# Optimization experiments

Hardware: AMD Instinct MI355X
Metric: run time of the kernel (lower is better)

Reference implementation:

```python
import jax, jax.numpy as jnp
import numpy as np
import hashlib

HIDDEN = 256
IN_SIZE = 32
ROUNDS = 64
BATCH = 8192


def _sha256_noise(nonces_u8: np.ndarray) -> np.ndarray:
    # Faithful to generate_noise: sha256 of the 32 nonce bytes gives 256 bits;
    # only indices i < 256 (byte_idx < 32) are set, so only round 0 has noise.
    B = nonces_u8.shape[0]
    noise = np.zeros((B, ROUNDS, HIDDEN), dtype=np.float32)
    for b in range(B):
        h = hashlib.sha256(nonces_u8[b].tobytes()).digest()
        bits = np.unpackbits(np.frombuffer(h, dtype=np.uint8), bitorder='little')
        noise[b, 0, :] = bits.astype(np.float32)
    return noise


def setup_inputs() -> dict:
    key = jax.random.key(0)
    k_nonce, k_mat = jax.random.split(key)
    nonces = jax.random.randint(k_nonce, (BATCH, IN_SIZE), 0, 256, dtype=jnp.int32)
    # Ternary round matrices in {-1, 0, 1}; original derives them from a
    # ChaCha20 keystream mod 3 minus 1 -- same distribution, different PRNG.
    matrices = (jax.random.randint(k_mat, (ROUNDS, HIDDEN, HIDDEN), 0, 3, dtype=jnp.int32) - 1).astype(jnp.float32)
    nonces_u8 = np.asarray(nonces).astype(np.uint8)
    noise = jnp.asarray(_sha256_noise(nonces_u8))  # [B, ROUNDS, HIDDEN]
    return {"nonces": nonces, "matrices": matrices, "noise": noise}


def reference(nonces, matrices, noise):
    B = nonces.shape[0]
    # Vectorized bit-unpack: x[b, i*8 + j] = (nonces[b, i] >> j) & 1
    bits = ((nonces[:, :, None] >> jnp.arange(8, dtype=jnp.int32)) & 1)
    x = bits.reshape(B, IN_SIZE * 8).astype(jnp.float32)  # [B, 256]

    noise_r = jnp.swapaxes(noise, 0, 1)  # [ROUNDS, B, HIDDEN]

    def step(x, mn):
        M, n = mn
        # torch: fmod(matmul(M, x.T).T + noise_r, 2.0) == fmod(x @ M.T + n, 2)
        return jnp.fmod(x @ M.T + n, 2.0), None

    x, _ = jax.lax.scan(step, x, (matrices, noise_r))
    return x
```

## Files before the change

kernel.cpp:

```cpp
#include <hip/hip_runtime.h>


#define HIDDEN 256
#define ROUNDS 64
#define ROWS_PER_BLOCK 32

typedef __attribute__((ext_vector_type(4))) int int4v;

struct alignas(16) C16 { char b[16]; };

__global__ void prep_B(const float* __restrict__ M, char* __restrict__ Bfrag) {
    int cid = blockIdx.x * blockDim.x + threadIdx.x;
    int lane = cid & 63;
    int q    = (cid >> 6) & 3;
    int t    = (cid >> 8) & 15;
    int r    = cid >> 12;
    int h  = 16 * t + (lane & 15);
    int k0 = 64 * q + (lane >> 4) * 16;
    const float* src = M + (((size_t)r * 256 + h) * 256 + k0);
    C16 w;
#pragma unroll
    for (int j = 0; j < 16; j++) w.b[j] = (char)src[j];
    *(C16*)(Bfrag + (size_t)cid * 16) = w;
}

__global__ __launch_bounds__(512, 2) void tenshash_main(
    const int*   __restrict__ nonces,
    const char*  __restrict__ Bfrag,
    const float* __restrict__ noise,
    float*       __restrict__ out)
{
    __shared__ alignas(16) char xbuf[2][ROWS_PER_BLOCK * HIDDEN];

    const int tid  = threadIdx.x;
    const int lane = tid & 63;
    const int wave = tid >> 6;
    const int lane15 = lane & 15;
    const int quad   = lane >> 4;
    const int b0 = blockIdx.x * ROWS_PER_BLOCK;

    {
        int m = tid >> 4;
        int c = tid & 15;
        int n0 = nonces[(b0 + m) * 32 + 2 * c];
        int n1 = nonces[(b0 + m) * 32 + 2 * c + 1];
        C16 w;
#pragma unroll
        for (int j = 0; j < 8; j++) w.b[j]     = (char)((n0 >> j) & 1);
#pragma unroll
        for (int j = 0; j < 8; j++) w.b[8 + j] = (char)((n1 >> j) & 1);
        int off = m * 256 + ((c ^ (m & 15)) * 16);
        *(C16*)&xbuf[0][off] = w;
    }
    __syncthreads();

    for (int r = 0; r < ROUNDS; r++) {
        const char* xcur = xbuf[r & 1];
        char*       xnxt = xbuf[(r & 1) ^ 1];

        int4v a[2][4];
#pragma unroll
        for (int mt = 0; mt < 2; mt++) {
            int m = 16 * mt + lane15;
#pragma unroll
            for (int kt = 0; kt < 4; kt++) {
                int c = 4 * kt + quad;
                int off = m * 256 + ((c ^ lane15) * 16);
                a[mt][kt] = *(const int4v*)&xcur[off];
            }
        }

        int4v acc[2][2];
#pragma unroll
        for (int nt = 0; nt < 2; nt++) {
            int t = wave * 2 + nt;
            const int4v* bptr = (const int4v*)Bfrag
                              + (((size_t)r * 16 + t) * 4) * 64 + lane;
            int4v b[4];
#pragma unroll
            for (int q = 0; q < 4; q++) b[q] = bptr[q * 64];
#pragma unroll
            for (int mt = 0; mt < 2; mt++) {
                int4v c = {0, 0, 0, 0};
#pragma unroll
                for (int q = 0; q < 4; q++)
                    c = __builtin_amdgcn_mfma_i32_16x16x64_i8(a[mt][q], b[q], c, 0, 0, 0);
                acc[nt][mt] = c;
            }
        }

#pragma unroll
        for (int nt = 0; nt < 2; nt++) {
            int t = wave * 2 + nt;
            int h = 16 * t + lane15;
#pragma unroll
            for (int mt = 0; mt < 2; mt++) {
#pragma unroll
                for (int reg = 0; reg < 4; reg++) {
                    int row = 16 * mt + 4 * quad + reg;
                    int v = acc[nt][mt][reg];
                    if (r == 0)
                        v += (int)noise[(size_t)(b0 + row) * (ROUNDS * 256) + h];
                    int m2 = v % 2;
                    if (r < ROUNDS - 1) {
                        int off = row * 256 + ((t ^ (row & 15)) * 16) + lane15;
                        xnxt[off] = (char)m2;
                    } else {
                        out[(size_t)(b0 + row) * 256 + h] = (float)m2;
                    }
                }
            }
        }
        __syncthreads();
    }
}

extern "C" void kernel_launch(void* const* d_in, const int* in_sizes, int n_in,
                              void* d_out, int out_size, void* d_ws, size_t ws_size,
                              hipStream_t stream) {
    const int*   nonces   = (const int*)d_in[0];
    const float* matrices = (const float*)d_in[1];
    const float* noise    = (const float*)d_in[2];
    float* out = (float*)d_out;
    char* Bfrag = (char*)d_ws;

    prep_B<<<1024, 256, 0, stream>>>(matrices, Bfrag);
    tenshash_main<<<256, 512, 0, stream>>>(nonces, Bfrag, noise, out);
}
```

Baseline: 654.4 us.

## Prefetch next-round matrix fragments into registers and swap MFMA operand roles

The main loop now loads the next round's ternary matrix fragments from global memory into a second register set while the current round's MFMAs run, double-buffering them across an unrolled pair of rounds. The matrix becomes the A operand and the activations the B operand, so each lane's output holds four consecutive hidden values. That lets results be written to shared memory as packed 32-bit stores, and the final output and round-0 noise as float4 vectors, instead of scalar byte and float accesses. prep_A also reads the source floats as float4. Holding the extra fragments costs more registers, which may strain the 2-blocks-per-CU launch bound.

```diff
diff --git a/kernel.cpp b/kernel.cpp
--- a/kernel.cpp
+++ b/kernel.cpp
@@ -1,43 +1,121 @@
 #include <hip/hip_runtime.h>
 
 
-#define HIDDEN 256
 #define ROUNDS 64
-#define ROWS_PER_BLOCK 32
+#define ROWS   32
 
-typedef __attribute__((ext_vector_type(4))) int int4v;
+typedef __attribute__((ext_vector_type(4))) int    int4v;
+typedef __attribute__((ext_vector_type(4))) float  float4v;
 
 struct alignas(16) C16 { char b[16]; };
 
-__global__ void prep_B(const float* __restrict__ M, char* __restrict__ Bfrag) {
-    int cid = blockIdx.x * blockDim.x + threadIdx.x;
+__global__ void prep_A(const float* __restrict__ M, char* __restrict__ A) {
+    int cid  = blockIdx.x * blockDim.x + threadIdx.x;
     int lane = cid & 63;
-    int q    = (cid >> 6) & 3;
-    int t    = (cid >> 8) & 15;
+    int kt   = (cid >> 6) & 3;
+    int ht   = (cid >> 8) & 15;
     int r    = cid >> 12;
-    int h  = 16 * t + (lane & 15);
-    int k0 = 64 * q + (lane >> 4) * 16;
-    const float* src = M + (((size_t)r * 256 + h) * 256 + k0);
+    int h  = 16 * ht + (lane & 15);
+    int k0 = 64 * kt + (lane >> 4) * 16;
+    const float4v* src = (const float4v*)(M + ((size_t)(r * 256 + h) * 256 + k0));
     C16 w;
 #pragma unroll
-    for (int j = 0; j < 16; j++) w.b[j] = (char)src[j];
-    *(C16*)(Bfrag + (size_t)cid * 16) = w;
+    for (int p = 0; p < 4; p++) {
+        float4v f = src[p];
+#pragma unroll
+        for (int e = 0; e < 4; e++) w.b[4 * p + e] = (char)f[e];
+    }
+    *(C16*)(A + (size_t)cid * 16) = w;
+}
+
+__device__ __forceinline__ void round_body(
+    int r, bool last, bool pre,
+    const char* __restrict__ xc, char* __restrict__ xn,
+    int4v (&a)[2][4], int4v (&an)[2][4],
+    const int4v* __restrict__ Abase,
+    const float* __restrict__ noise, float* __restrict__ out,
+    int b0, int lane, int wave)
+{
+    const int l15  = lane & 15;
+    const int quad = lane >> 4;
+
+    int4v b[2][4];
+#pragma unroll
+    for (int bt = 0; bt < 2; bt++) {
+        int row = 16 * bt + l15;
+#pragma unroll
+        for (int kt = 0; kt < 4; kt++) {
+            int c = 4 * kt + quad;
+            b[bt][kt] = *(const int4v*)&xc[row * 256 + ((c ^ l15) * 16)];
+        }
+    }
+
+    if (pre) {
+#pragma unroll
+        for (int i = 0; i < 2; i++) {
+            int ht = 2 * wave + i;
+#pragma unroll
+            for (int kt = 0; kt < 4; kt++)
+                an[i][kt] = Abase[(size_t)((((r + 1) * 16 + ht) * 4 + kt) * 64) + lane];
+        }
+    }
+
+    int4v acc[2][2];
+#pragma unroll
+    for (int i = 0; i < 2; i++)
+#pragma unroll
+        for (int bt = 0; bt < 2; bt++) {
+            int4v c = {0, 0, 0, 0};
+#pragma unroll
+            for (int kt = 0; kt < 4; kt++)
+                c = __builtin_amdgcn_mfma_i32_16x16x64_i8(a[i][kt], b[bt][kt], c, 0, 0, 0);
+            acc[i][bt] = c;
+        }
+
+#pragma unroll
+    for (int i = 0; i < 2; i++) {
+        int ht = 2 * wave + i;
+#pragma unroll
+        for (int bt = 0; bt < 2; bt++) {
+            int bb = 16 * bt + l15;
+            int4v v = acc[i][bt];
+            if (r == 0) {
+                float4v nz = *(const float4v*)&noise[(size_t)(b0 + bb) * (ROUNDS * 256)
+                                                     + 16 * ht + 4 * quad];
+#pragma unroll
+                for (int e = 0; e < 4; e++) v[e] += (int)nz[e];
+            }
+            if (!last) {
+                unsigned p = 0;
+#pragma unroll
+                for (int e = 0; e < 4; e++) {
+                    int m2 = v[e] % 2;
+                    p |= ((unsigned)(m2 & 0xff)) << (8 * e);
+                }
+                *(unsigned*)&xn[bb * 256 + ((ht ^ l15) * 16) + 4 * quad] = p;
+            } else {
+                float4v o;
+#pragma unroll
+                for (int e = 0; e < 4; e++) o[e] = (float)(v[e] % 2);
+                *(float4v*)&out[(size_t)(b0 + bb) * 256 + 16 * ht + 4 * quad] = o;
+            }
+        }
+    }
+    __syncthreads();
 }
 
 __global__ __launch_bounds__(512, 2) void tenshash_main(
     const int*   __restrict__ nonces,
-    const char*  __restrict__ Bfrag,
+    const char*  __restrict__ Afrag,
     const float* __restrict__ noise,
     float*       __restrict__ out)
 {
-    __shared__ alignas(16) char xbuf[2][ROWS_PER_BLOCK * HIDDEN];
+    __shared__ alignas(16) char xbuf[2][ROWS * 256];
 
     const int tid  = threadIdx.x;
     const int lane = tid & 63;
     const int wave = tid >> 6;
-    const int lane15 = lane & 15;
-    const int quad   = lane >> 4;
-    const int b0 = blockIdx.x * ROWS_PER_BLOCK;
+    const int b0 = blockIdx.x * ROWS;
 
     {
         int m = tid >> 4;
@@ -49,69 +127,26 @@
         for (int j = 0; j < 8; j++) w.b[j]     = (char)((n0 >> j) & 1);
 #pragma unroll
         for (int j = 0; j < 8; j++) w.b[8 + j] = (char)((n1 >> j) & 1);
-        int off = m * 256 + ((c ^ (m & 15)) * 16);
-        *(C16*)&xbuf[0][off] = w;
+        *(C16*)&xbuf[0][m * 256 + ((c ^ (m & 15)) * 16)] = w;
+    }
+
+    const int4v* Abase = (const int4v*)Afrag;
+    int4v aA[2][4], aB[2][4];
+#pragma unroll
+    for (int i = 0; i < 2; i++) {
+        int ht = 2 * wave + i;
+#pragma unroll
+        for (int kt = 0; kt < 4; kt++)
+            aA[i][kt] = Abase[(size_t)(((ht) * 4 + kt) * 64) + lane];
     }
     __syncthreads();
 
-    for (int r = 0; r < ROUNDS; r++) {
-        const char* xcur = xbuf[r & 1];
-        char*       xnxt = xbuf[(r & 1) ^ 1];
-
-        int4v a[2][4];
-#pragma unroll
-        for (int mt = 0; mt < 2; mt++) {
-            int m = 16 * mt + lane15;
-#pragma unroll
-            for (int kt = 0; kt < 4; kt++) {
-                int c = 4 * kt + quad;
-                int off = m * 256 + ((c ^ lane15) * 16);
-                a[mt][kt] = *(const int4v*)&xcur[off];
-            }
-        }
-
-        int4v acc[2][2];
-#pragma unroll
-        for (int nt = 0; nt < 2; nt++) {
-            int t = wave * 2 + nt;
-            const int4v* bptr = (const int4v*)Bfrag
-                              + (((size_t)r * 16 + t) * 4) * 64 + lane;
-            int4v b[4];
-#pragma unroll
-            for (int q = 0; q < 4; q++) b[q] = bptr[q * 64];
-#pragma unroll
-            for (int mt = 0; mt < 2; mt++) {
-                int4v c = {0, 0, 0, 0};
-#pragma unroll
-                for (int q = 0; q < 4; q++)
-                    c = __builtin_amdgcn_mfma_i32_16x16x64_i8(a[mt][q], b[q], c, 0, 0, 0);
-                acc[nt][mt] = c;
-            }
-        }
-
-#pragma unroll
-        for (int nt = 0; nt < 2; nt++) {
-            int t = wave * 2 + nt;
-            int h = 16 * t + lane15;
-#pragma unroll
-            for (int mt = 0; mt < 2; mt++) {
-#pragma unroll
-                for (int reg = 0; reg < 4; reg++) {
-                    int row = 16 * mt + 4 * quad + reg;
-                    int v = acc[nt][mt][reg];
-                    if (r == 0)
-                        v += (int)noise[(size_t)(b0 + row) * (ROUNDS * 256) + h];
-                    int m2 = v % 2;
-                    if (r < ROUNDS - 1) {
-                        int off = row * 256 + ((t ^ (row & 15)) * 16) + lane15;
-                        xnxt[off] = (char)m2;
-                    } else {
-                        out[(size_t)(b0 + row) * 256 + h] = (float)m2;
-                    }
-                }
-            }
-        }
-        __syncthreads();
+    for (int rr = 0; rr < ROUNDS / 2; rr++) {
+        int r0 = 2 * rr;
+        round_body(r0,     false,            true,
+                   xbuf[0], xbuf[1], aA, aB, Abase, noise, out, b0, lane, wave);
+        round_body(r0 + 1, r0 + 1 == ROUNDS - 1, rr < ROUNDS / 2 - 1,
+                   xbuf[1], xbuf[0], aB, aA, Abase, noise, out, b0, lane, wave);
     }
 }
 
@@ -121,9 +156,9 @@
     const int*   nonces   = (const int*)d_in[0];
     const float* matrices = (const float*)d_in[1];
     const float* noise    = (const float*)d_in[2];
-    float* out = (float*)d_out;
-    char* Bfrag = (char*)d_ws;
+    float* out  = (float*)d_out;
+    char* Afrag = (char*)d_ws;
 
-    prep_B<<<1024, 256, 0, stream>>>(matrices, Bfrag);
-    tenshash_main<<<256, 512, 0, stream>>>(nonces, Bfrag, noise, out);
+    prep_A<<<1024, 256, 0, stream>>>(matrices, Afrag);
+    tenshash_main<<<256, 512, 0, stream>>>(nonces, Afrag, noise, out);
 }
```

Result: faster. 635.6 us (-2.9%).
